# Performance work log

Measured on AMD Instinct MI355X. Metric: run time of the kernel, lower is better.

Reference implementation:

```python
import jax, jax.numpy as jnp
import numpy as np

B, N, D, E, ET, L = 2, 50000, 64, 400000, 200000, 6
R_STRUCT = 4
EPS = 1e-5


def _ln(x, g, b):
    m = jnp.mean(x, axis=-1, keepdims=True)
    v = jnp.mean((x - m) ** 2, axis=-1, keepdims=True)
    return (x - m) * jax.lax.rsqrt(v + EPS) * g + b


def _nbf(boundary, src, dst, rel_e_fn, W, b, g, beta):
    # One RelNBFNet / TextRelNBFNet stack of GeneralizedRelationalConv layers:
    #   distmult message, sum aggregation with boundary self-loop message,
    #   linear([x, agg]) -> layernorm -> relu, short_cut residual.
    # boundary: [B, N, D]
    x = boundary
    for i in range(W.shape[0]):
        msg = x[:, src, :] * rel_e_fn(i)                    # [B, E, D]
        agg = jnp.zeros_like(x).at[:, dst, :].add(msg) + boundary
        h = jnp.concatenate([x, agg], axis=-1) @ W[i] + b[i]
        h = jax.nn.relu(_ln(h, g[i], beta[i]))
        x = h + x                                           # short_cut
    return x


def setup_inputs() -> dict:
    key = jax.random.key(0)
    ks = jax.random.split(key, 16)
    s = 0.05
    return {
        "rel_text_init": jax.random.normal(ks[0], (N, D), jnp.float32),
        "struct_rel": jax.random.normal(ks[1], (L, R_STRUCT, D), jnp.float32) * s,
        "struct_W": jax.random.normal(ks[2], (L, 2 * D, D), jnp.float32) * s,
        "struct_b": jnp.zeros((L, D), jnp.float32),
        "struct_g": jnp.ones((L, D), jnp.float32),
        "struct_beta": jnp.zeros((L, D), jnp.float32),
        "text_rel": jax.random.normal(ks[3], (L, 1, D), jnp.float32) * s,
        "text_W": jax.random.normal(ks[4], (L, 2 * D, D), jnp.float32) * s,
        "text_b": jnp.zeros((L, D), jnp.float32),
        "text_g": jnp.ones((L, D), jnp.float32),
        "text_beta": jnp.zeros((L, D), jnp.float32),
        "fuse_W1": jax.random.normal(ks[5], (2 * D, D), jnp.float32) * s,
        "fuse_b1": jnp.zeros((D,), jnp.float32),
        "fuse_W2": jax.random.normal(ks[6], (D, D), jnp.float32) * s,
        "fuse_b2": jnp.zeros((D,), jnp.float32),
        "h_index": jax.random.randint(ks[7], (B,), 0, N),
        "edge_index": jax.random.randint(ks[8], (2, E), 0, N),
        "edge_type": jax.random.randint(ks[9], (E,), 0, R_STRUCT),
        "text_edge_index": jax.random.randint(ks[10], (2, ET), 0, N),
    }


def reference(rel_text_init, struct_rel, struct_W, struct_b, struct_g, struct_beta,
              text_rel, text_W, text_b, text_g, text_beta,
              fuse_W1, fuse_b1, fuse_W2, fuse_b2,
              h_index, edge_index, edge_type, text_edge_index):
    # struct branch: boundary = indicator at query relation node
    boundary_s = jnp.zeros((B, N, D), rel_text_init.dtype).at[jnp.arange(B), h_index].add(1.0)
    h = _nbf(boundary_s, edge_index[0], edge_index[1],
             lambda i: struct_rel[i][edge_type],
             struct_W, struct_b, struct_g, struct_beta)
    # text branch: boundary = text-derived init features, single relation type
    boundary_t = jnp.broadcast_to(rel_text_init[None], (B, N, D))
    z = _nbf(boundary_t, text_edge_index[0], text_edge_index[1],
             lambda i: text_rel[i, 0][None, None, :],
             text_W, text_b, text_g, text_beta)
    # mlp fusion (alpha = 1.0)
    f = jax.nn.relu(jnp.concatenate([h, z], axis=-1) @ fuse_W1 + fuse_b1)
    return f @ fuse_W2 + fuse_b2
```

## Files before the change

### kernel.cpp

```cpp
#include <hip/hip_runtime.h>


#define FMA4R(v, wbase, R0, R1, R2, R3) do {                                  \
    const float4* _w = (const float4*)(wbase); float4 _t;                     \
    _t=_w[0]; R0.x=fmaf(v,_t.x,R0.x); R0.y=fmaf(v,_t.y,R0.y); R0.z=fmaf(v,_t.z,R0.z); R0.w=fmaf(v,_t.w,R0.w); \
    _t=_w[1]; R1.x=fmaf(v,_t.x,R1.x); R1.y=fmaf(v,_t.y,R1.y); R1.z=fmaf(v,_t.z,R1.z); R1.w=fmaf(v,_t.w,R1.w); \
    _t=_w[2]; R2.x=fmaf(v,_t.x,R2.x); R2.y=fmaf(v,_t.y,R2.y); R2.z=fmaf(v,_t.z,R2.z); R2.w=fmaf(v,_t.w,R2.w); \
    _t=_w[3]; R3.x=fmaf(v,_t.x,R3.x); R3.y=fmaf(v,_t.y,R3.y); R3.z=fmaf(v,_t.z,R3.z); R3.w=fmaf(v,_t.w,R3.w); \
} while (0)

#define FMA16(v, wbase) do {                                                  \
    FMA4R(v, (wbase),      A0, A1, A2, A3);                                   \
    FMA4R(v, (wbase) + 16, A4, A5, A6, A7);                                   \
    FMA4R(v, (wbase) + 32, A8, A9, A10, A11);                                 \
    FMA4R(v, (wbase) + 48, A12, A13, A14, A15);                               \
} while (0)

#define SUM4(Ai) ((Ai.x + Ai.y) + (Ai.z + Ai.w))
#define VAR4(Ai) do { float _c;                                               \
    _c = Ai.x - m; vs = fmaf(_c, _c, vs); _c = Ai.y - m; vs = fmaf(_c, _c, vs); \
    _c = Ai.z - m; vs = fmaf(_c, _c, vs); _c = Ai.w - m; vs = fmaf(_c, _c, vs); \
} while (0)

__global__ __launch_bounds__(256) void k_init_onehot(
    float* __restrict__ x, const int* __restrict__ h_index, int N, int total)
{
    int idx = blockIdx.x * 256 + threadIdx.x;
    if (idx >= total) return;
    int row = idx >> 6;
    int b = row / N;
    int n = row - b * N;
    x[idx] = (n == h_index[b]) ? 1.0f : 0.0f;
}

__global__ __launch_bounds__(256) void k_hist(
    const int* __restrict__ dst, int* __restrict__ cnt, int E)
{
    int e = blockIdx.x * 256 + threadIdx.x;
    if (e < E) atomicAdd(&cnt[dst[e]], 1);
}

__global__ __launch_bounds__(1024) void k_scan(
    const int* __restrict__ cnt, int* __restrict__ off, int n)
{
    __shared__ int wpre[16];
    __shared__ int total_s;
    __shared__ int carry_s;
    int tid = threadIdx.x, lane = tid & 63, w = tid >> 6;
    if (tid == 0) { carry_s = 0; off[0] = 0; }
    __syncthreads();
    for (int base = 0; base < n; base += 1024) {
        int i = base + tid;
        int v = (i < n) ? cnt[i] : 0;
        int s = v;
        #pragma unroll
        for (int d = 1; d < 64; d <<= 1) {
            int t = __shfl_up(s, d);
            if (lane >= d) s += t;
        }
        __shared__ int wsum[16];
        if (lane == 63) wsum[w] = s;
        __syncthreads();
        if (w == 0 && lane < 16) {
            int ws = wsum[lane];
            int p = ws;
            #pragma unroll
            for (int d = 1; d < 16; d <<= 1) {
                int t = __shfl_up(p, d);
                if (lane >= d) p += t;
            }
            wpre[lane] = p - ws;
            if (lane == 15) total_s = p;
        }
        __syncthreads();
        int carry = carry_s;
        if (i < n) off[i + 1] = carry + wpre[w] + s;
        __syncthreads();
        if (tid == 0) carry_s = carry + total_s;
        __syncthreads();
    }
}

__global__ __launch_bounds__(256) void k_fill(
    const int* __restrict__ src, const int* __restrict__ dst,
    const int* __restrict__ etype,
    const int* __restrict__ off, int* __restrict__ cnt,
    int* __restrict__ packed, int E)
{
    int e = blockIdx.x * 256 + threadIdx.x;
    if (e >= E) return;
    int d = dst[e];
    int pos = off[d] + atomicSub(&cnt[d], 1) - 1;
    int ty = etype ? etype[e] : 0;
    packed[pos] = src[e] | (ty << 27);
}

__global__ __launch_bounds__(256) void k_gather_struct2(
    const float* __restrict__ x, float* __restrict__ agg,
    const int* __restrict__ off, const int* __restrict__ packed,
    const float* __restrict__ rel,
    const int* __restrict__ h_index,
    int N)
{
    int n = (blockIdx.x * 256 + threadIdx.x) >> 6;
    int lane = threadIdx.x & 63;
    if (n >= N) return;
    float r0 = rel[lane], r1 = rel[64 + lane];
    float r2 = rel[128 + lane], r3 = rel[192 + lane];
    const float* x0 = x;
    const float* x1 = x + (size_t)N * 64;
    float acc0 = (n == h_index[0]) ? 1.0f : 0.0f;
    float acc1 = (n == h_index[1]) ? 1.0f : 0.0f;
    int p0 = __builtin_amdgcn_readfirstlane(off[n]);
    int p1 = __builtin_amdgcn_readfirstlane(off[n + 1]);
    int p = p0;
    for (; p + 4 <= p1; p += 4) {
        int pka = __builtin_amdgcn_readfirstlane(packed[p + 0]);
        int pkb = __builtin_amdgcn_readfirstlane(packed[p + 1]);
        int pkc = __builtin_amdgcn_readfirstlane(packed[p + 2]);
        int pkd = __builtin_amdgcn_readfirstlane(packed[p + 3]);
        int sa = pka & 0x03FFFFFF, ta = pka >> 27;
        int sb = pkb & 0x03FFFFFF, tb = pkb >> 27;
        int sc = pkc & 0x03FFFFFF, tc = pkc >> 27;
        int sd = pkd & 0x03FFFFFF, td = pkd >> 27;
        float ra = (ta < 2) ? (ta == 0 ? r0 : r1) : (ta == 2 ? r2 : r3);
        float rb = (tb < 2) ? (tb == 0 ? r0 : r1) : (tb == 2 ? r2 : r3);
        float rc = (tc < 2) ? (tc == 0 ? r0 : r1) : (tc == 2 ? r2 : r3);
        float rd = (td < 2) ? (td == 0 ? r0 : r1) : (td == 2 ? r2 : r3);
        float a0 = x0[(size_t)sa * 64 + lane], a1 = x1[(size_t)sa * 64 + lane];
        float b0 = x0[(size_t)sb * 64 + lane], b1 = x1[(size_t)sb * 64 + lane];
        float c0 = x0[(size_t)sc * 64 + lane], c1 = x1[(size_t)sc * 64 + lane];
        float d0 = x0[(size_t)sd * 64 + lane], d1 = x1[(size_t)sd * 64 + lane];
        acc0 = fmaf(a0, ra, acc0); acc1 = fmaf(a1, ra, acc1);
        acc0 = fmaf(b0, rb, acc0); acc1 = fmaf(b1, rb, acc1);
        acc0 = fmaf(c0, rc, acc0); acc1 = fmaf(c1, rc, acc1);
        acc0 = fmaf(d0, rd, acc0); acc1 = fmaf(d1, rd, acc1);
    }
    for (; p < p1; ++p) {
        int pk = __builtin_amdgcn_readfirstlane(packed[p]);
        int s = pk & 0x03FFFFFF, ty = pk >> 27;
        float r = (ty < 2) ? (ty == 0 ? r0 : r1) : (ty == 2 ? r2 : r3);
        float v0 = x0[(size_t)s * 64 + lane], v1 = x1[(size_t)s * 64 + lane];
        acc0 = fmaf(v0, r, acc0); acc1 = fmaf(v1, r, acc1);
    }
    agg[(size_t)n * 64 + lane] = acc0;
    agg[(size_t)(N + n) * 64 + lane] = acc1;
}

__global__ __launch_bounds__(256) void k_gather_struct_gen(
    const float* __restrict__ x, float* __restrict__ agg,
    const int* __restrict__ off, const int* __restrict__ packed,
    const float* __restrict__ rel, const int* __restrict__ h_index,
    int N, int BN)
{
    int wid = (blockIdx.x * 256 + threadIdx.x) >> 6;
    int lane = threadIdx.x & 63;
    if (wid >= BN) return;
    int b = wid / N;
    int n = wid - b * N;
    float r0 = rel[lane], r1 = rel[64 + lane];
    float r2 = rel[128 + lane], r3 = rel[192 + lane];
    const float* xb = x + (size_t)b * N * 64;
    float acc = (n == h_index[b]) ? 1.0f : 0.0f;
    int p0 = off[n], p1 = off[n + 1];
    for (int p = p0; p < p1; ++p) {
        int pk = packed[p];
        int s = pk & 0x03FFFFFF, ty = pk >> 27;
        float r = (ty < 2) ? (ty == 0 ? r0 : r1) : (ty == 2 ? r2 : r3);
        acc = fmaf(xb[(size_t)s * 64 + lane], r, acc);
    }
    agg[(size_t)wid * 64 + lane] = acc;
}

__global__ __launch_bounds__(256) void k_gather_text(
    const float* __restrict__ x, float* __restrict__ agg,
    const int* __restrict__ off, const int* __restrict__ packed,
    const float* __restrict__ rel,
    const float* __restrict__ init,
    int N)
{
    int n = (blockIdx.x * 256 + threadIdx.x) >> 6;
    int lane = threadIdx.x & 63;
    if (n >= N) return;
    float r = rel[lane];
    float acc = init[(size_t)n * 64 + lane];
    int p0 = __builtin_amdgcn_readfirstlane(off[n]);
    int p1 = __builtin_amdgcn_readfirstlane(off[n + 1]);
    int p = p0;
    float acc2 = 0.f;
    for (; p + 4 <= p1; p += 4) {
        int sa = __builtin_amdgcn_readfirstlane(packed[p + 0]);
        int sb = __builtin_amdgcn_readfirstlane(packed[p + 1]);
        int sc = __builtin_amdgcn_readfirstlane(packed[p + 2]);
        int sd = __builtin_amdgcn_readfirstlane(packed[p + 3]);
        float a = x[(size_t)sa * 64 + lane];
        float b = x[(size_t)sb * 64 + lane];
        float c = x[(size_t)sc * 64 + lane];
        float d = x[(size_t)sd * 64 + lane];
        acc = fmaf(a, r, acc);  acc2 = fmaf(b, r, acc2);
        acc = fmaf(c, r, acc);  acc2 = fmaf(d, r, acc2);
    }
    for (; p < p1; ++p) {
        int s = __builtin_amdgcn_readfirstlane(packed[p]);
        acc = fmaf(x[(size_t)s * 64 + lane], r, acc);
    }
    agg[(size_t)n * 64 + lane] = acc + acc2;
}

__global__ __launch_bounds__(256) void k_update(
    const float* __restrict__ W,
    const float* __restrict__ bias, const float* __restrict__ g,
    const float* __restrict__ beta,
    float* __restrict__ x, const float* __restrict__ agg, int rows)
{
    __shared__ float Wl[128 * 64];
    __shared__ float bl[64], gl[64], bel[64];
    int tid = threadIdx.x;
    {
        const float4* W4 = (const float4*)W;
        float4* Wl4 = (float4*)Wl;
        #pragma unroll
        for (int i = 0; i < 8; ++i) Wl4[tid + i * 256] = W4[tid + i * 256];
        if (tid < 64) { bl[tid] = bias[tid]; gl[tid] = g[tid]; bel[tid] = beta[tid]; }
    }
    __syncthreads();

    int gt = blockIdx.x * 256 + tid;
    int row = gt >> 2;
    int jc = (gt & 3) * 16;
    if (row >= rows) return;
    const float* xr = x + (size_t)row * 64;
    const float* ar = agg + (size_t)row * 64;

    const float4* bj = (const float4*)(bl + jc);
    float4 A0 = bj[0], A1 = bj[1], A2 = bj[2], A3 = bj[3];

    #pragma unroll
    for (int kb = 0; kb < 64; kb += 4) {
        float4 iv = *(const float4*)(xr + kb);
        FMA4R(iv.x, Wl + (kb + 0) * 64 + jc, A0, A1, A2, A3);
        FMA4R(iv.y, Wl + (kb + 1) * 64 + jc, A0, A1, A2, A3);
        FMA4R(iv.z, Wl + (kb + 2) * 64 + jc, A0, A1, A2, A3);
        FMA4R(iv.w, Wl + (kb + 3) * 64 + jc, A0, A1, A2, A3);
    }
    #pragma unroll
    for (int kb = 0; kb < 64; kb += 4) {
        float4 iv = *(const float4*)(ar + kb);
        FMA4R(iv.x, Wl + (64 + kb + 0) * 64 + jc, A0, A1, A2, A3);
        FMA4R(iv.y, Wl + (64 + kb + 1) * 64 + jc, A0, A1, A2, A3);
        FMA4R(iv.z, Wl + (64 + kb + 2) * 64 + jc, A0, A1, A2, A3);
        FMA4R(iv.w, Wl + (64 + kb + 3) * 64 + jc, A0, A1, A2, A3);
    }

    float ls = SUM4(A0) + SUM4(A1) + SUM4(A2) + SUM4(A3);
    ls += __shfl_xor(ls, 1);
    ls += __shfl_xor(ls, 2);
    float m = ls * (1.0f / 64.0f);
    float vs = 0.f;
    VAR4(A0); VAR4(A1); VAR4(A2); VAR4(A3);
    vs += __shfl_xor(vs, 1);
    vs += __shfl_xor(vs, 2);
    float inv = rsqrtf(vs * (1.0f / 64.0f) + 1e-5f);

    float* xw = x + (size_t)row * 64 + jc;
    const float4* gg4 = (const float4*)(gl + jc);
    const float4* bb4 = (const float4*)(bel + jc);
    const float4* xv4 = (const float4*)(xr + jc);
    #define OUTC(Aj, c) do {                                                  \
        float4 xv = xv4[c]; float4 gg = gg4[c]; float4 bb = bb4[c];           \
        float4 y;                                                             \
        y.x = fmaxf((Aj.x - m) * inv * gg.x + bb.x, 0.f) + xv.x;              \
        y.y = fmaxf((Aj.y - m) * inv * gg.y + bb.y, 0.f) + xv.y;              \
        y.z = fmaxf((Aj.z - m) * inv * gg.z + bb.z, 0.f) + xv.z;              \
        y.w = fmaxf((Aj.w - m) * inv * gg.w + bb.w, 0.f) + xv.w;              \
        ((float4*)xw)[c] = y; } while (0)
    OUTC(A0, 0); OUTC(A1, 1); OUTC(A2, 2); OUTC(A3, 3);
    #undef OUTC
}

__global__ __launch_bounds__(256) void k_fuse(
    const float* __restrict__ W1, const float* __restrict__ b1,
    const float* __restrict__ W2, const float* __restrict__ b2,
    float* __restrict__ out, const float* __restrict__ z, int N, int rows)
{
    __shared__ float W1l[128 * 64];
    __shared__ float W2l[64 * 64];
    __shared__ float b1l[64], b2l[64];
    int tid = threadIdx.x;
    {
        const float4* Wa = (const float4*)W1;
        float4* Wla = (float4*)W1l;
        #pragma unroll
        for (int i = 0; i < 8; ++i) Wla[tid + i * 256] = Wa[tid + i * 256];
        const float4* Wb = (const float4*)W2;
        float4* Wlb = (float4*)W2l;
        #pragma unroll
        for (int i = 0; i < 4; ++i) Wlb[tid + i * 256] = Wb[tid + i * 256];
        if (tid < 64) { b1l[tid] = b1[tid]; b2l[tid] = b2[tid]; }
    }
    __syncthreads();

    int row = blockIdx.x * 256 + tid;
    if (row >= rows) return;
    int n = row % N;
    const float* hr = out + (size_t)row * 64;
    const float* zr = z + (size_t)n * 64;

    const float4* b1l4 = (const float4*)b1l;
    float4 A0 = b1l4[0],  A1 = b1l4[1],  A2 = b1l4[2],  A3 = b1l4[3];
    float4 A4 = b1l4[4],  A5 = b1l4[5],  A6 = b1l4[6],  A7 = b1l4[7];
    float4 A8 = b1l4[8],  A9 = b1l4[9],  A10 = b1l4[10], A11 = b1l4[11];
    float4 A12 = b1l4[12], A13 = b1l4[13], A14 = b1l4[14], A15 = b1l4[15];

    #pragma unroll
    for (int kc = 0; kc < 64; kc += 4) {
        float4 iv = *(const float4*)(hr + kc);
        FMA16(iv.x, W1l + (kc + 0) * 64);
        FMA16(iv.y, W1l + (kc + 1) * 64);
        FMA16(iv.z, W1l + (kc + 2) * 64);
        FMA16(iv.w, W1l + (kc + 3) * 64);
    }
    #pragma unroll
    for (int kc = 0; kc < 64; kc += 4) {
        float4 iv = *(const float4*)(zr + kc);
        FMA16(iv.x, W1l + (64 + kc + 0) * 64);
        FMA16(iv.y, W1l + (64 + kc + 1) * 64);
        FMA16(iv.z, W1l + (64 + kc + 2) * 64);
        FMA16(iv.w, W1l + (64 + kc + 3) * 64);
    }
    #define RELU4(Ai) do { Ai.x = fmaxf(Ai.x, 0.f); Ai.y = fmaxf(Ai.y, 0.f); \
                           Ai.z = fmaxf(Ai.z, 0.f); Ai.w = fmaxf(Ai.w, 0.f); } while (0)
    RELU4(A0);  RELU4(A1);  RELU4(A2);  RELU4(A3);
    RELU4(A4);  RELU4(A5);  RELU4(A6);  RELU4(A7);
    RELU4(A8);  RELU4(A9);  RELU4(A10); RELU4(A11);
    RELU4(A12); RELU4(A13); RELU4(A14); RELU4(A15);
    #undef RELU4

    float* ow = out + (size_t)row * 64;
    #pragma unroll
    for (int jc = 0; jc < 64; jc += 16) {
        const float4* bb4 = (const float4*)(b2l + jc);
        float4 O0 = bb4[0], O1 = bb4[1], O2 = bb4[2], O3 = bb4[3];
        #define KS(Ai, kb) do {                                               \
            FMA4R(Ai.x, W2l + (kb + 0) * 64 + jc, O0, O1, O2, O3);            \
            FMA4R(Ai.y, W2l + (kb + 1) * 64 + jc, O0, O1, O2, O3);            \
            FMA4R(Ai.z, W2l + (kb + 2) * 64 + jc, O0, O1, O2, O3);            \
            FMA4R(Ai.w, W2l + (kb + 3) * 64 + jc, O0, O1, O2, O3); } while (0)
        KS(A0, 0);   KS(A1, 4);   KS(A2, 8);   KS(A3, 12);
        KS(A4, 16);  KS(A5, 20);  KS(A6, 24);  KS(A7, 28);
        KS(A8, 32);  KS(A9, 36);  KS(A10, 40); KS(A11, 44);
        KS(A12, 48); KS(A13, 52); KS(A14, 56); KS(A15, 60);
        #undef KS
        float4* ow4 = (float4*)(ow + jc);
        ow4[0] = O0; ow4[1] = O1; ow4[2] = O2; ow4[3] = O3;
    }
}

extern "C" void kernel_launch(void* const* d_in, const int* in_sizes, int n_in,
                              void* d_out, int out_size, void* d_ws, size_t ws_size,
                              hipStream_t stream)
{
    const float* rel_text_init = (const float*)d_in[0];
    const float* struct_rel    = (const float*)d_in[1];
    const float* struct_W      = (const float*)d_in[2];
    const float* struct_b      = (const float*)d_in[3];
    const float* struct_g      = (const float*)d_in[4];
    const float* struct_beta   = (const float*)d_in[5];
    const float* text_rel      = (const float*)d_in[6];
    const float* text_W        = (const float*)d_in[7];
    const float* text_b        = (const float*)d_in[8];
    const float* text_g        = (const float*)d_in[9];
    const float* text_beta     = (const float*)d_in[10];
    const float* fuse_W1       = (const float*)d_in[11];
    const float* fuse_b1       = (const float*)d_in[12];
    const float* fuse_W2       = (const float*)d_in[13];
    const float* fuse_b2       = (const float*)d_in[14];
    const int*   h_index       = (const int*)d_in[15];
    const int*   edge_index    = (const int*)d_in[16];
    const int*   edge_type     = (const int*)d_in[17];
    const int*   text_edge_idx = (const int*)d_in[18];

    const int B  = in_sizes[15];
    const int N  = in_sizes[0] / 64;
    const int E  = in_sizes[17];
    const int ET = in_sizes[18] / 2;
    const int L  = in_sizes[3] / 64;
    const int R  = in_sizes[1] / (L * 64);

    const int* src  = edge_index;
    const int* dst  = edge_index + E;
    const int* tsrc = text_edge_idx;
    const int* tdst = text_edge_idx + ET;

    float* x_t   = (float*)d_ws;
    float* agg_t = x_t + (size_t)N * 64;
    float* agg_s = agg_t + (size_t)N * 64;
    int*   cnt_s = (int*)(agg_s + (size_t)B * N * 64);
    int*   off_s = cnt_s + N;
    int*   pk_s  = off_s + N + 1;
    int*   cnt_t = pk_s + E;
    int*   off_t = cnt_t + N;
    int*   pk_t  = off_t + N + 1;

    float* x_s = (float*)d_out;

    const size_t nd  = (size_t)N * 64;
    const int rows_s = B * N;
    const int tot_s  = rows_s * 64;

    const int gb_init   = (tot_s + 255) / 256;
    const int gb_e      = (E + 255) / 256;
    const int gb_et     = (ET + 255) / 256;
    const int gb_wave_n = (N * 64 + 255) / 256;
    const int gb_upd_s  = (rows_s * 4 + 255) / 256;
    const int gb_upd_t  = (N * 4 + 255) / 256;
    const int gb_fuse   = (rows_s + 255) / 256;

    hipMemsetAsync(cnt_s, 0, (size_t)N * 4, stream);
    hipMemsetAsync(cnt_t, 0, (size_t)N * 4, stream);
    k_hist<<<gb_e, 256, 0, stream>>>(dst, cnt_s, E);
    k_hist<<<gb_et, 256, 0, stream>>>(tdst, cnt_t, ET);
    k_scan<<<1, 1024, 0, stream>>>(cnt_s, off_s, N);
    k_scan<<<1, 1024, 0, stream>>>(cnt_t, off_t, N);
    k_fill<<<gb_e, 256, 0, stream>>>(src, dst, edge_type, off_s, cnt_s, pk_s, E);
    k_fill<<<gb_et, 256, 0, stream>>>(tsrc, tdst, nullptr, off_t, cnt_t, pk_t, ET);

    k_init_onehot<<<gb_init, 256, 0, stream>>>(x_s, h_index, N, tot_s);
    for (int i = 0; i < L; ++i) {
        if (B == 2) {
            k_gather_struct2<<<gb_wave_n, 256, 0, stream>>>(
                x_s, agg_s, off_s, pk_s,
                struct_rel + (size_t)i * R * 64, h_index, N);
        } else {
            k_gather_struct_gen<<<(rows_s * 64 + 255) / 256, 256, 0, stream>>>(
                x_s, agg_s, off_s, pk_s,
                struct_rel + (size_t)i * R * 64, h_index, N, rows_s);
        }
        k_update<<<gb_upd_s, 256, 0, stream>>>(
            struct_W + (size_t)i * 128 * 64, struct_b + i * 64,
            struct_g + i * 64, struct_beta + i * 64, x_s, agg_s, rows_s);
    }

    hipMemcpyAsync(x_t, rel_text_init, nd * sizeof(float),
                   hipMemcpyDeviceToDevice, stream);
    for (int i = 0; i < L; ++i) {
        k_gather_text<<<gb_wave_n, 256, 0, stream>>>(
            x_t, agg_t, off_t, pk_t,
            text_rel + (size_t)i * 64, rel_text_init, N);
        k_update<<<gb_upd_t, 256, 0, stream>>>(
            text_W + (size_t)i * 128 * 64, text_b + i * 64,
            text_g + i * 64, text_beta + i * 64, x_t, agg_t, N);
    }

    k_fuse<<<gb_fuse, 256, 0, stream>>>(
        fuse_W1, fuse_b1, fuse_W2, fuse_b2, x_s, x_t, N, rows_s);
}
```

Measured before the change: 863.7 us.

## Parallelize CSR scan, batch edge index loads via shuffles, split fusion MLP rows

```diff
diff --git a/kernel.cpp b/kernel.cpp
--- a/kernel.cpp
+++ b/kernel.cpp
@@ -9,18 +9,13 @@
     _t=_w[3]; R3.x=fmaf(v,_t.x,R3.x); R3.y=fmaf(v,_t.y,R3.y); R3.z=fmaf(v,_t.z,R3.z); R3.w=fmaf(v,_t.w,R3.w); \
 } while (0)
 
-#define FMA16(v, wbase) do {                                                  \
-    FMA4R(v, (wbase),      A0, A1, A2, A3);                                   \
-    FMA4R(v, (wbase) + 16, A4, A5, A6, A7);                                   \
-    FMA4R(v, (wbase) + 32, A8, A9, A10, A11);                                 \
-    FMA4R(v, (wbase) + 48, A12, A13, A14, A15);                               \
-} while (0)
-
 #define SUM4(Ai) ((Ai.x + Ai.y) + (Ai.z + Ai.w))
 #define VAR4(Ai) do { float _c;                                               \
     _c = Ai.x - m; vs = fmaf(_c, _c, vs); _c = Ai.y - m; vs = fmaf(_c, _c, vs); \
     _c = Ai.z - m; vs = fmaf(_c, _c, vs); _c = Ai.w - m; vs = fmaf(_c, _c, vs); \
 } while (0)
+
+#define RSEL(ty) (((ty) < 2) ? ((ty) == 0 ? r0 : r1) : ((ty) == 2 ? r2 : r3))
 
 __global__ __launch_bounds__(256) void k_init_onehot(
     float* __restrict__ x, const int* __restrict__ h_index, int N, int total)
@@ -40,45 +35,73 @@
     if (e < E) atomicAdd(&cnt[dst[e]], 1);
 }
 
-__global__ __launch_bounds__(1024) void k_scan(
-    const int* __restrict__ cnt, int* __restrict__ off, int n)
-{
-    __shared__ int wpre[16];
-    __shared__ int total_s;
-    __shared__ int carry_s;
+__global__ __launch_bounds__(1024) void k_scan_blk(
+    const int* __restrict__ cnt, int* __restrict__ off,
+    int* __restrict__ bsum, int n)
+{
+    __shared__ int wsum[16], wpre[16], tot;
     int tid = threadIdx.x, lane = tid & 63, w = tid >> 6;
-    if (tid == 0) { carry_s = 0; off[0] = 0; }
+    int i = blockIdx.x * 1024 + tid;
+    int v = (i < n) ? cnt[i] : 0;
+    int s = v;
+    #pragma unroll
+    for (int d = 1; d < 64; d <<= 1) {
+        int t = __shfl_up(s, d);
+        if (lane >= d) s += t;
+    }
+    if (lane == 63) wsum[w] = s;
     __syncthreads();
-    for (int base = 0; base < n; base += 1024) {
-        int i = base + tid;
-        int v = (i < n) ? cnt[i] : 0;
-        int s = v;
+    if (w == 0 && lane < 16) {
+        int ws = wsum[lane];
+        int p = ws;
         #pragma unroll
-        for (int d = 1; d < 64; d <<= 1) {
-            int t = __shfl_up(s, d);
-            if (lane >= d) s += t;
-        }
-        __shared__ int wsum[16];
-        if (lane == 63) wsum[w] = s;
-        __syncthreads();
-        if (w == 0 && lane < 16) {
-            int ws = wsum[lane];
-            int p = ws;
-            #pragma unroll
-            for (int d = 1; d < 16; d <<= 1) {
-                int t = __shfl_up(p, d);
-                if (lane >= d) p += t;
-            }
-            wpre[lane] = p - ws;
-            if (lane == 15) total_s = p;
-        }
-        __syncthreads();
-        int carry = carry_s;
-        if (i < n) off[i + 1] = carry + wpre[w] + s;
-        __syncthreads();
-        if (tid == 0) carry_s = carry + total_s;
-        __syncthreads();
-    }
+        for (int d = 1; d < 16; d <<= 1) {
+            int t = __shfl_up(p, d);
+            if (lane >= d) p += t;
+        }
+        wpre[lane] = p - ws;
+        if (lane == 15) tot = p;
+    }
+    __syncthreads();
+    if (i < n) off[i + 1] = wpre[w] + s;
+    if (tid == 0) {
+        bsum[blockIdx.x] = tot;
+        if (blockIdx.x == 0) off[0] = 0;
+    }
+}
+
+__global__ __launch_bounds__(1024) void k_scan_top(int* __restrict__ bsum, int nb)
+{
+    __shared__ int wsum[16], wpre[16];
+    int tid = threadIdx.x, lane = tid & 63, w = tid >> 6;
+    int v = (tid < nb) ? bsum[tid] : 0;
+    int s = v;
+    #pragma unroll
+    for (int d = 1; d < 64; d <<= 1) {
+        int t = __shfl_up(s, d);
+        if (lane >= d) s += t;
+    }
+    if (lane == 63) wsum[w] = s;
+    __syncthreads();
+    if (w == 0 && lane < 16) {
+        int ws = wsum[lane];
+        int p = ws;
+        #pragma unroll
+        for (int d = 1; d < 16; d <<= 1) {
+            int t = __shfl_up(p, d);
+            if (lane >= d) p += t;
+        }
+        wpre[lane] = p - ws;
+    }
+    __syncthreads();
+    if (tid < nb) bsum[tid] = wpre[w] + s - v;
+}
+
+__global__ __launch_bounds__(1024) void k_scan_add(
+    const int* __restrict__ bsum, int* __restrict__ off, int n)
+{
+    int i = blockIdx.x * 1024 + threadIdx.x;
+    if (i < n) off[i + 1] += bsum[blockIdx.x];
 }
 
 __global__ __launch_bounds__(256) void k_fill(
@@ -113,35 +136,34 @@
     float acc1 = (n == h_index[1]) ? 1.0f : 0.0f;
     int p0 = __builtin_amdgcn_readfirstlane(off[n]);
     int p1 = __builtin_amdgcn_readfirstlane(off[n + 1]);
-    int p = p0;
-    for (; p + 4 <= p1; p += 4) {
-        int pka = __builtin_amdgcn_readfirstlane(packed[p + 0]);
-        int pkb = __builtin_amdgcn_readfirstlane(packed[p + 1]);
-        int pkc = __builtin_amdgcn_readfirstlane(packed[p + 2]);
-        int pkd = __builtin_amdgcn_readfirstlane(packed[p + 3]);
-        int sa = pka & 0x03FFFFFF, ta = pka >> 27;
-        int sb = pkb & 0x03FFFFFF, tb = pkb >> 27;
-        int sc = pkc & 0x03FFFFFF, tc = pkc >> 27;
-        int sd = pkd & 0x03FFFFFF, td = pkd >> 27;
-        float ra = (ta < 2) ? (ta == 0 ? r0 : r1) : (ta == 2 ? r2 : r3);
-        float rb = (tb < 2) ? (tb == 0 ? r0 : r1) : (tb == 2 ? r2 : r3);
-        float rc = (tc < 2) ? (tc == 0 ? r0 : r1) : (tc == 2 ? r2 : r3);
-        float rd = (td < 2) ? (td == 0 ? r0 : r1) : (td == 2 ? r2 : r3);
-        float a0 = x0[(size_t)sa * 64 + lane], a1 = x1[(size_t)sa * 64 + lane];
-        float b0 = x0[(size_t)sb * 64 + lane], b1 = x1[(size_t)sb * 64 + lane];
-        float c0 = x0[(size_t)sc * 64 + lane], c1 = x1[(size_t)sc * 64 + lane];
-        float d0 = x0[(size_t)sd * 64 + lane], d1 = x1[(size_t)sd * 64 + lane];
-        acc0 = fmaf(a0, ra, acc0); acc1 = fmaf(a1, ra, acc1);
-        acc0 = fmaf(b0, rb, acc0); acc1 = fmaf(b1, rb, acc1);
-        acc0 = fmaf(c0, rc, acc0); acc1 = fmaf(c1, rc, acc1);
-        acc0 = fmaf(d0, rd, acc0); acc1 = fmaf(d1, rd, acc1);
-    }
-    for (; p < p1; ++p) {
-        int pk = __builtin_amdgcn_readfirstlane(packed[p]);
-        int s = pk & 0x03FFFFFF, ty = pk >> 27;
-        float r = (ty < 2) ? (ty == 0 ? r0 : r1) : (ty == 2 ? r2 : r3);
-        float v0 = x0[(size_t)s * 64 + lane], v1 = x1[(size_t)s * 64 + lane];
-        acc0 = fmaf(v0, r, acc0); acc1 = fmaf(v1, r, acc1);
+    for (int p = p0; p < p1; p += 64) {
+        int myPk = (p + lane < p1) ? packed[p + lane] : 0;
+        int cnt = min(p1 - p, 64);
+        int i = 0;
+        for (; i + 4 <= cnt; i += 4) {
+            int pka = __shfl(myPk, i + 0), pkb = __shfl(myPk, i + 1);
+            int pkc = __shfl(myPk, i + 2), pkd = __shfl(myPk, i + 3);
+            int sa = pka & 0x03FFFFFF, ta = pka >> 27;
+            int sb = pkb & 0x03FFFFFF, tb = pkb >> 27;
+            int sc = pkc & 0x03FFFFFF, tc = pkc >> 27;
+            int sd = pkd & 0x03FFFFFF, td = pkd >> 27;
+            float ra = RSEL(ta), rb = RSEL(tb), rc = RSEL(tc), rd = RSEL(td);
+            float a0 = x0[(size_t)sa * 64 + lane], a1 = x1[(size_t)sa * 64 + lane];
+            float b0 = x0[(size_t)sb * 64 + lane], b1 = x1[(size_t)sb * 64 + lane];
+            float c0 = x0[(size_t)sc * 64 + lane], c1 = x1[(size_t)sc * 64 + lane];
+            float d0 = x0[(size_t)sd * 64 + lane], d1 = x1[(size_t)sd * 64 + lane];
+            acc0 = fmaf(a0, ra, acc0); acc1 = fmaf(a1, ra, acc1);
+            acc0 = fmaf(b0, rb, acc0); acc1 = fmaf(b1, rb, acc1);
+            acc0 = fmaf(c0, rc, acc0); acc1 = fmaf(c1, rc, acc1);
+            acc0 = fmaf(d0, rd, acc0); acc1 = fmaf(d1, rd, acc1);
+        }
+        for (; i < cnt; ++i) {
+            int pk = __shfl(myPk, i);
+            int s = pk & 0x03FFFFFF, ty = pk >> 27;
+            float r = RSEL(ty);
+            acc0 = fmaf(x0[(size_t)s * 64 + lane], r, acc0);
+            acc1 = fmaf(x1[(size_t)s * 64 + lane], r, acc1);
+        }
     }
     agg[(size_t)n * 64 + lane] = acc0;
     agg[(size_t)(N + n) * 64 + lane] = acc1;
@@ -166,8 +188,7 @@
     for (int p = p0; p < p1; ++p) {
         int pk = packed[p];
         int s = pk & 0x03FFFFFF, ty = pk >> 27;
-        float r = (ty < 2) ? (ty == 0 ? r0 : r1) : (ty == 2 ? r2 : r3);
-        acc = fmaf(xb[(size_t)s * 64 + lane], r, acc);
+        acc = fmaf(xb[(size_t)s * 64 + lane], RSEL(ty), acc);
     }
     agg[(size_t)wid * 64 + lane] = acc;
 }
@@ -184,25 +205,27 @@
     if (n >= N) return;
     float r = rel[lane];
     float acc = init[(size_t)n * 64 + lane];
+    float acc2 = 0.f;
     int p0 = __builtin_amdgcn_readfirstlane(off[n]);
     int p1 = __builtin_amdgcn_readfirstlane(off[n + 1]);
-    int p = p0;
-    float acc2 = 0.f;
-    for (; p + 4 <= p1; p += 4) {
-        int sa = __builtin_amdgcn_readfirstlane(packed[p + 0]);
-        int sb = __builtin_amdgcn_readfirstlane(packed[p + 1]);
-        int sc = __builtin_amdgcn_readfirstlane(packed[p + 2]);
-        int sd = __builtin_amdgcn_readfirstlane(packed[p + 3]);
-        float a = x[(size_t)sa * 64 + lane];
-        float b = x[(size_t)sb * 64 + lane];
-        float c = x[(size_t)sc * 64 + lane];
-        float d = x[(size_t)sd * 64 + lane];
-        acc = fmaf(a, r, acc);  acc2 = fmaf(b, r, acc2);
-        acc = fmaf(c, r, acc);  acc2 = fmaf(d, r, acc2);
-    }
-    for (; p < p1; ++p) {
-        int s = __builtin_amdgcn_readfirstlane(packed[p]);
-        acc = fmaf(x[(size_t)s * 64 + lane], r, acc);
+    for (int p = p0; p < p1; p += 64) {
+        int myPk = (p + lane < p1) ? packed[p + lane] : 0;
+        int cnt = min(p1 - p, 64);
+        int i = 0;
+        for (; i + 4 <= cnt; i += 4) {
+            int sa = __shfl(myPk, i + 0), sb = __shfl(myPk, i + 1);
+            int sc = __shfl(myPk, i + 2), sd = __shfl(myPk, i + 3);
+            float a = x[(size_t)sa * 64 + lane];
+            float b = x[(size_t)sb * 64 + lane];
+            float c = x[(size_t)sc * 64 + lane];
+            float d = x[(size_t)sd * 64 + lane];
+            acc = fmaf(a, r, acc);  acc2 = fmaf(b, r, acc2);
+            acc = fmaf(c, r, acc);  acc2 = fmaf(d, r, acc2);
+        }
+        for (; i < cnt; ++i) {
+            int s = __shfl(myPk, i);
+            acc = fmaf(x[(size_t)s * 64 + lane], r, acc);
+        }
     }
     agg[(size_t)n * 64 + lane] = acc + acc2;
 }
@@ -300,60 +323,75 @@
     }
     __syncthreads();
 
-    int row = blockIdx.x * 256 + tid;
+    int gt = blockIdx.x * 256 + tid;
+    int row = gt >> 2;
+    int q = gt & 3;
+    int jc = q * 16;
     if (row >= rows) return;
     int n = row % N;
     const float* hr = out + (size_t)row * 64;
     const float* zr = z + (size_t)n * 64;
-
-    const float4* b1l4 = (const float4*)b1l;
-    float4 A0 = b1l4[0],  A1 = b1l4[1],  A2 = b1l4[2],  A3 = b1l4[3];
-    float4 A4 = b1l4[4],  A5 = b1l4[5],  A6 = b1l4[6],  A7 = b1l4[7];
-    float4 A8 = b1l4[8],  A9 = b1l4[9],  A10 = b1l4[10], A11 = b1l4[11];
-    float4 A12 = b1l4[12], A13 = b1l4[13], A14 = b1l4[14], A15 = b1l4[15];
-
-    #pragma unroll
-    for (int kc = 0; kc < 64; kc += 4) {
-        float4 iv = *(const float4*)(hr + kc);
-        FMA16(iv.x, W1l + (kc + 0) * 64);
-        FMA16(iv.y, W1l + (kc + 1) * 64);
-        FMA16(iv.z, W1l + (kc + 2) * 64);
-        FMA16(iv.w, W1l + (kc + 3) * 64);
-    }
-    #pragma unroll
-    for (int kc = 0; kc < 64; kc += 4) {
-        float4 iv = *(const float4*)(zr + kc);
-        FMA16(iv.x, W1l + (64 + kc + 0) * 64);
-        FMA16(iv.y, W1l + (64 + kc + 1) * 64);
-        FMA16(iv.z, W1l + (64 + kc + 2) * 64);
-        FMA16(iv.w, W1l + (64 + kc + 3) * 64);
-    }
-    #define RELU4(Ai) do { Ai.x = fmaxf(Ai.x, 0.f); Ai.y = fmaxf(Ai.y, 0.f); \
-                           Ai.z = fmaxf(Ai.z, 0.f); Ai.w = fmaxf(Ai.w, 0.f); } while (0)
-    RELU4(A0);  RELU4(A1);  RELU4(A2);  RELU4(A3);
-    RELU4(A4);  RELU4(A5);  RELU4(A6);  RELU4(A7);
-    RELU4(A8);  RELU4(A9);  RELU4(A10); RELU4(A11);
-    RELU4(A12); RELU4(A13); RELU4(A14); RELU4(A15);
-    #undef RELU4
-
-    float* ow = out + (size_t)row * 64;
-    #pragma unroll
-    for (int jc = 0; jc < 64; jc += 16) {
-        const float4* bb4 = (const float4*)(b2l + jc);
-        float4 O0 = bb4[0], O1 = bb4[1], O2 = bb4[2], O3 = bb4[3];
-        #define KS(Ai, kb) do {                                               \
-            FMA4R(Ai.x, W2l + (kb + 0) * 64 + jc, O0, O1, O2, O3);            \
-            FMA4R(Ai.y, W2l + (kb + 1) * 64 + jc, O0, O1, O2, O3);            \
-            FMA4R(Ai.z, W2l + (kb + 2) * 64 + jc, O0, O1, O2, O3);            \
-            FMA4R(Ai.w, W2l + (kb + 3) * 64 + jc, O0, O1, O2, O3); } while (0)
-        KS(A0, 0);   KS(A1, 4);   KS(A2, 8);   KS(A3, 12);
-        KS(A4, 16);  KS(A5, 20);  KS(A6, 24);  KS(A7, 28);
-        KS(A8, 32);  KS(A9, 36);  KS(A10, 40); KS(A11, 44);
-        KS(A12, 48); KS(A13, 52); KS(A14, 56); KS(A15, 60);
-        #undef KS
-        float4* ow4 = (float4*)(ow + jc);
-        ow4[0] = O0; ow4[1] = O1; ow4[2] = O2; ow4[3] = O3;
-    }
+    int lane = tid & 63;
+
+    const float4* bj = (const float4*)(b1l + jc);
+    float4 F0 = bj[0], F1 = bj[1], F2 = bj[2], F3 = bj[3];
+    #pragma unroll
+    for (int kb = 0; kb < 64; kb += 4) {
+        float4 iv = *(const float4*)(hr + kb);
+        FMA4R(iv.x, W1l + (kb + 0) * 64 + jc, F0, F1, F2, F3);
+        FMA4R(iv.y, W1l + (kb + 1) * 64 + jc, F0, F1, F2, F3);
+        FMA4R(iv.z, W1l + (kb + 2) * 64 + jc, F0, F1, F2, F3);
+        FMA4R(iv.w, W1l + (kb + 3) * 64 + jc, F0, F1, F2, F3);
+    }
+    #pragma unroll
+    for (int kb = 0; kb < 64; kb += 4) {
+        float4 iv = *(const float4*)(zr + kb);
+        FMA4R(iv.x, W1l + (64 + kb + 0) * 64 + jc, F0, F1, F2, F3);
+        FMA4R(iv.y, W1l + (64 + kb + 1) * 64 + jc, F0, F1, F2, F3);
+        FMA4R(iv.z, W1l + (64 + kb + 2) * 64 + jc, F0, F1, F2, F3);
+        FMA4R(iv.w, W1l + (64 + kb + 3) * 64 + jc, F0, F1, F2, F3);
+    }
+    F0.x = fmaxf(F0.x, 0.f); F0.y = fmaxf(F0.y, 0.f); F0.z = fmaxf(F0.z, 0.f); F0.w = fmaxf(F0.w, 0.f);
+    F1.x = fmaxf(F1.x, 0.f); F1.y = fmaxf(F1.y, 0.f); F1.z = fmaxf(F1.z, 0.f); F1.w = fmaxf(F1.w, 0.f);
+    F2.x = fmaxf(F2.x, 0.f); F2.y = fmaxf(F2.y, 0.f); F2.z = fmaxf(F2.z, 0.f); F2.w = fmaxf(F2.w, 0.f);
+    F3.x = fmaxf(F3.x, 0.f); F3.y = fmaxf(F3.y, 0.f); F3.z = fmaxf(F3.z, 0.f); F3.w = fmaxf(F3.w, 0.f);
+
+    const float4* bj2 = (const float4*)(b2l + jc);
+    float4 O0 = bj2[0], O1 = bj2[1], O2 = bj2[2], O3 = bj2[3];
+    int srcLane = (lane & ~3) | ((q + 1) & 3);
+    #pragma unroll
+    for (int s = 0; s < 4; ++s) {
+        int c = (q + s) & 3;
+        const float* w2 = W2l + (c * 16) * 64 + jc;
+        FMA4R(F0.x, w2 + 0 * 64,  O0, O1, O2, O3);
+        FMA4R(F0.y, w2 + 1 * 64,  O0, O1, O2, O3);
+        FMA4R(F0.z, w2 + 2 * 64,  O0, O1, O2, O3);
+        FMA4R(F0.w, w2 + 3 * 64,  O0, O1, O2, O3);
+        FMA4R(F1.x, w2 + 4 * 64,  O0, O1, O2, O3);
+        FMA4R(F1.y, w2 + 5 * 64,  O0, O1, O2, O3);
+        FMA4R(F1.z, w2 + 6 * 64,  O0, O1, O2, O3);
+        FMA4R(F1.w, w2 + 7 * 64,  O0, O1, O2, O3);
+        FMA4R(F2.x, w2 + 8 * 64,  O0, O1, O2, O3);
+        FMA4R(F2.y, w2 + 9 * 64,  O0, O1, O2, O3);
+        FMA4R(F2.z, w2 + 10 * 64, O0, O1, O2, O3);
+        FMA4R(F2.w, w2 + 11 * 64, O0, O1, O2, O3);
+        FMA4R(F3.x, w2 + 12 * 64, O0, O1, O2, O3);
+        FMA4R(F3.y, w2 + 13 * 64, O0, O1, O2, O3);
+        FMA4R(F3.z, w2 + 14 * 64, O0, O1, O2, O3);
+        FMA4R(F3.w, w2 + 15 * 64, O0, O1, O2, O3);
+        if (s < 3) {
+            F0.x = __shfl(F0.x, srcLane); F0.y = __shfl(F0.y, srcLane);
+            F0.z = __shfl(F0.z, srcLane); F0.w = __shfl(F0.w, srcLane);
+            F1.x = __shfl(F1.x, srcLane); F1.y = __shfl(F1.y, srcLane);
+            F1.z = __shfl(F1.z, srcLane); F1.w = __shfl(F1.w, srcLane);
+            F2.x = __shfl(F2.x, srcLane); F2.y = __shfl(F2.y, srcLane);
+            F2.z = __shfl(F2.z, srcLane); F2.w = __shfl(F2.w, srcLane);
+            F3.x = __shfl(F3.x, srcLane); F3.y = __shfl(F3.y, srcLane);
+            F3.z = __shfl(F3.z, srcLane); F3.w = __shfl(F3.w, srcLane);
+        }
+    }
+    float4* ow4 = (float4*)(out + (size_t)row * 64 + jc);
+    ow4[0] = O0; ow4[1] = O1; ow4[2] = O2; ow4[3] = O3;
 }
 
 extern "C" void kernel_launch(void* const* d_in, const int* in_sizes, int n_in,
@@ -401,12 +439,15 @@
     int*   cnt_t = pk_s + E;
     int*   off_t = cnt_t + N;
     int*   pk_t  = off_t + N + 1;
+    int*   bsum_s = pk_t + ET;
+    int*   bsum_t = bsum_s + 1024;
 
     float* x_s = (float*)d_out;
 
     const size_t nd  = (size_t)N * 64;
     const int rows_s = B * N;
     const int tot_s  = rows_s * 64;
+    const int nb     = (N + 1023) / 1024;
 
     const int gb_init   = (tot_s + 255) / 256;
     const int gb_e      = (E + 255) / 256;
@@ -414,14 +455,18 @@
     const int gb_wave_n = (N * 64 + 255) / 256;
     const int gb_upd_s  = (rows_s * 4 + 255) / 256;
     const int gb_upd_t  = (N * 4 + 255) / 256;
-    const int gb_fuse   = (rows_s + 255) / 256;
+    const int gb_fuse   = (rows_s * 4 + 255) / 256;
 
     hipMemsetAsync(cnt_s, 0, (size_t)N * 4, stream);
     hipMemsetAsync(cnt_t, 0, (size_t)N * 4, stream);
     k_hist<<<gb_e, 256, 0, stream>>>(dst, cnt_s, E);
     k_hist<<<gb_et, 256, 0, stream>>>(tdst, cnt_t, ET);
-    k_scan<<<1, 1024, 0, stream>>>(cnt_s, off_s, N);
-    k_scan<<<1, 1024, 0, stream>>>(cnt_t, off_t, N);
+    k_scan_blk<<<nb, 1024, 0, stream>>>(cnt_s, off_s, bsum_s, N);
+    k_scan_blk<<<nb, 1024, 0, stream>>>(cnt_t, off_t, bsum_t, N);
+    k_scan_top<<<1, 1024, 0, stream>>>(bsum_s, nb);
+    k_scan_top<<<1, 1024, 0, stream>>>(bsum_t, nb);
+    k_scan_add<<<nb, 1024, 0, stream>>>(bsum_s, off_s, N);
+    k_scan_add<<<nb, 1024, 0, stream>>>(bsum_t, off_t, N);
     k_fill<<<gb_e, 256, 0, stream>>>(src, dst, edge_type, off_s, cnt_s, pk_s, E);
     k_fill<<<gb_et, 256, 0, stream>>>(tsrc, tdst, nullptr, off_t, cnt_t, pk_t, ET);
 
```

New measurement: 800.2 us. 7.3% less time.
